# Kernel optimization log

Hardware: AMD Instinct MI355X
Metric: run time of the kernel (lower is better)

Reference implementation:

```python
import jax, jax.numpy as jnp
import numpy as np

EPS = 1e-5  # BatchNorm eps (PyTorch default)


def gcn_conv(x, edge_index, W, b):
    """PyG GCNConv with add_self_loops=True, normalize=True.
    out[j] = sum_{(i->j)} x_w[i] / sqrt(deg_i * deg_j) + x_w[j] / deg_j + b,
    deg_j = 1 + in-degree(j) (self-loop included)."""
    n = x.shape[0]
    src, dst = edge_index[0], edge_index[1]
    ones = jnp.ones(src.shape[0], x.dtype)
    deg = 1.0 + jax.ops.segment_sum(ones, dst, num_segments=n)  # [n]
    dis = jax.lax.rsqrt(deg)
    xw = x @ W  # [n, out]
    msg = xw[src] * (dis[src] * dis[dst])[:, None]  # gather + per-edge norm
    agg = jax.ops.segment_sum(msg, dst, num_segments=n)  # scatter-add
    agg = agg + xw * (1.0 / deg)[:, None]  # self-loop term
    return agg + b


def bn_relu(x, gamma, beta):
    # BatchNorm1d over the node dim (training-mode batch stats) + ReLU
    mean = x.mean(axis=0)
    var = x.var(axis=0)
    return jax.nn.relu((x - mean) * jax.lax.rsqrt(var + EPS) * gamma + beta)


def wireframe_gnn(x, edge_index, layers, fcW, fcb):
    feats = [x]
    h = x
    for (W, b, g, be) in layers:  # fixed small n_layers loop
        h = bn_relu(gcn_conv(h, edge_index, W, b), g, be)
        feats.append(h)
    cat = jnp.concatenate(feats, axis=1)
    return jax.nn.relu(cat @ fcW + fcb)


N_L, N_J = 50000, 25000
D_FC, NF = 1024, 256
E_L, E_J = 400000, 100000
L_LAB, J_LAB = 10, 3


def setup_inputs() -> dict:
    key = jax.random.key(0)
    ks = iter(jax.random.split(key, 48))
    p = lambda shape: (jax.random.normal(next(ks), shape, jnp.float32) * 0.02)
    inp = {}
    inp["line_features"] = jax.random.normal(next(ks), (N_L, D_FC), jnp.float32)
    inp["junction_features"] = jax.random.normal(next(ks), (N_J, NF), jnp.float32)
    inp["line_edge_index"] = jax.random.randint(next(ks), (2, E_L), 0, N_L, jnp.int64)
    inp["junction_edge_index"] = jax.random.randint(next(ks), (2, E_J), 0, N_J, jnp.int64)
    # line GNN: 1024 -> 512 -> 256, concat 1792 -> fc 1024
    inp["lg_W1"], inp["lg_b1"] = p((D_FC, D_FC // 2)), p((D_FC // 2,))
    inp["lg_g1"], inp["lg_be1"] = jnp.ones(D_FC // 2, jnp.float32), jnp.zeros(D_FC // 2, jnp.float32)
    inp["lg_W2"], inp["lg_b2"] = p((D_FC // 2, D_FC // 4)), p((D_FC // 4,))
    inp["lg_g2"], inp["lg_be2"] = jnp.ones(D_FC // 4, jnp.float32), jnp.zeros(D_FC // 4, jnp.float32)
    cat_l = D_FC + D_FC // 2 + D_FC // 4  # 1792
    inp["lg_fcW"], inp["lg_fcb"] = p((cat_l, D_FC)), p((D_FC,))
    # fc_lines: 1024 -> 1024 -> 1024 -> L_LAB (dim_loi*n_pts1 == dim_fc == 1024)
    inp["fl_W1"], inp["fl_b1"] = p((D_FC, D_FC)), p((D_FC,))
    inp["fl_W2"], inp["fl_b2"] = p((D_FC, D_FC)), p((D_FC,))
    inp["fl_W3"], inp["fl_b3"] = p((D_FC, L_LAB)), p((L_LAB,))
    # junction GNN: 256 -> 128 -> 64, concat 448 -> fc 256
    inp["jg_W1"], inp["jg_b1"] = p((NF, NF // 2)), p((NF // 2,))
    inp["jg_g1"], inp["jg_be1"] = jnp.ones(NF // 2, jnp.float32), jnp.zeros(NF // 2, jnp.float32)
    inp["jg_W2"], inp["jg_b2"] = p((NF // 2, NF // 4)), p((NF // 4,))
    inp["jg_g2"], inp["jg_be2"] = jnp.ones(NF // 4, jnp.float32), jnp.zeros(NF // 4, jnp.float32)
    cat_j = NF + NF // 2 + NF // 4  # 448
    inp["jg_fcW"], inp["jg_fcb"] = p((cat_j, NF)), p((NF,))
    # fc_junction: 256 -> 64 -> J_LAB
    m = NF // 4
    inp["fj_W1"], inp["fj_b1"] = p((NF, m)), p((m,))
    inp["fj_W2"], inp["fj_b2"] = p((m, J_LAB)), p((J_LAB,))
    return inp


def reference(line_features, junction_features, line_edge_index, junction_edge_index,
              lg_W1, lg_b1, lg_g1, lg_be1, lg_W2, lg_b2, lg_g2, lg_be2, lg_fcW, lg_fcb,
              fl_W1, fl_b1, fl_W2, fl_b2, fl_W3, fl_b3,
              jg_W1, jg_b1, jg_g1, jg_be1, jg_W2, jg_b2, jg_g2, jg_be2, jg_fcW, jg_fcb,
              fj_W1, fj_b1, fj_W2, fj_b2):
    # line branch
    h = wireframe_gnn(line_features, line_edge_index,
                      [(lg_W1, lg_b1, lg_g1, lg_be1), (lg_W2, lg_b2, lg_g2, lg_be2)],
                      lg_fcW, lg_fcb)
    h = jax.nn.relu(h @ fl_W1 + fl_b1)
    h = jax.nn.relu(h @ fl_W2 + fl_b2)
    line_logits = h @ fl_W3 + fl_b3
    # junction branch
    g = wireframe_gnn(junction_features, junction_edge_index,
                      [(jg_W1, jg_b1, jg_g1, jg_be1), (jg_W2, jg_b2, jg_g2, jg_be2)],
                      jg_fcW, jg_fcb)
    g = jax.nn.relu(g @ fj_W1 + fj_b1)
    junction_logits = g @ fj_W2 + fj_b2
    return (line_logits, junction_logits)
```

## Files before the change

kernel.cpp:

```cpp
#include <hip/hip_runtime.h>
#include <stdint.h>
#include <stddef.h>

typedef _Float16 f16;
typedef _Float16 f16x8 __attribute__((ext_vector_type(8)));
typedef _Float16 f16x4_t __attribute__((ext_vector_type(4)));
typedef float floatx4 __attribute__((ext_vector_type(4)));

template <int N> struct F16Vec { typedef f16 type __attribute__((ext_vector_type(N))); };

#define BN_EPS 1e-5f

struct WtJob { const float* W; f16* Wt; int K; int N; int tN; int tilebase; };
struct WtBatch { WtJob j[12]; int njobs; int ntiles; };

__global__ void k_wt_tiled(WtBatch b) {
  __shared__ float T[32][33];
  int bt = blockIdx.x;
  int i = 0;
  #pragma unroll 1
  while (i + 1 < b.njobs && bt >= b.j[i + 1].tilebase) ++i;
  WtJob J = b.j[i];
  int t = bt - J.tilebase;
  int tr = t / J.tN, tc = t - tr * J.tN;
  int ty = threadIdx.x >> 5, tx = threadIdx.x & 31;
  #pragma unroll
  for (int s = 0; s < 32; s += 8) {
    int k = tr * 32 + ty + s, n = tc * 32 + tx;
    if (k < J.K && n < J.N) T[ty + s][tx] = J.W[(size_t)k * J.N + n];
  }
  __syncthreads();
  #pragma unroll
  for (int s = 0; s < 32; s += 8) {
    int n = tc * 32 + ty + s, k = tr * 32 + tx;
    if (n < J.N && k < J.K) J.Wt[(size_t)n * J.K + k] = (f16)T[tx][ty + s];
  }
}

__global__ void k_cvt_cols(const float* __restrict__ src, f16* __restrict__ dst,
                           int n, int c, int ldd, int coff) {
  int t = blockIdx.x * blockDim.x + threadIdx.x;
  int cq = c >> 2;
  if (t >= n * cq) return;
  int r = t / cq, j = (t - r * cq) << 2;
  float4 v = *(const float4*)(src + (size_t)r * c + j);
  f16x4_t o; o[0] = (f16)v.x; o[1] = (f16)v.y; o[2] = (f16)v.z; o[3] = (f16)v.w;
  *(f16x4_t*)(dst + (size_t)r * ldd + coff + j) = o;
}

__global__ void k_count2(const int* __restrict__ dL, int EL, int* __restrict__ cntL,
                         const int* __restrict__ dJ, int EJ, int* __restrict__ cntJ) {
  int t = blockIdx.x * blockDim.x + threadIdx.x;
  if (t < EL) atomicAdd(&cntL[dL[t]], 1);
  else if (t < EL + EJ) atomicAdd(&cntJ[dJ[t - EL]], 1);
}

__global__ void k_scan4(const int* __restrict__ cnt, int n, int* __restrict__ rowstart,
                        float* __restrict__ dis) {
  __shared__ int wsum[16];
  __shared__ int carry_s;
  int tid = threadIdx.x, lane = tid & 63, wv = tid >> 6;
  if (tid == 0) { carry_s = 0; rowstart[0] = 0; }
  __syncthreads();
  for (int base = 0; base < n; base += 4096) {
    int i4 = base + tid * 4;
    int4 c = {0, 0, 0, 0};
    if (i4 < n) c = *(const int4*)(cnt + i4);
    int s0 = c.x, s1 = s0 + c.y, s2 = s1 + c.z, s3 = s2 + c.w;
    int x = s3;
    #pragma unroll
    for (int off = 1; off < 64; off <<= 1) {
      int y = __shfl_up(x, off, 64);
      if (lane >= off) x += y;
    }
    if (lane == 63) wsum[wv] = x;
    __syncthreads();
    if (wv == 0) {
      int s = (lane < 16) ? wsum[lane] : 0;
      #pragma unroll
      for (int off = 1; off < 16; off <<= 1) {
        int y = __shfl_up(s, off, 64);
        if (lane >= off) s += y;
      }
      if (lane < 16) wsum[lane] = s;
    }
    __syncthreads();
    int waveoff = (wv == 0) ? 0 : wsum[wv - 1];
    int excl = (x - s3) + waveoff + carry_s;
    if (i4 < n) {
      rowstart[i4 + 1] = excl + s0;
      rowstart[i4 + 2] = excl + s1;
      rowstart[i4 + 3] = excl + s2;
      rowstart[i4 + 4] = excl + s3;
      dis[i4 + 0] = rsqrtf(1.0f + (float)c.x);
      dis[i4 + 1] = rsqrtf(1.0f + (float)c.y);
      dis[i4 + 2] = rsqrtf(1.0f + (float)c.z);
      dis[i4 + 3] = rsqrtf(1.0f + (float)c.w);
    }
    __syncthreads();
    if (tid == 1023) carry_s = excl + s3;
    __syncthreads();
  }
}

__global__ void k_fill2(const int* __restrict__ eiL, int EL, const int* __restrict__ rsL,
                        int* __restrict__ fillL, int* __restrict__ cixL,
                        const int* __restrict__ eiJ, int EJ, const int* __restrict__ rsJ,
                        int* __restrict__ fillJ, int* __restrict__ cixJ) {
  int t = blockIdx.x * blockDim.x + threadIdx.x;
  if (t < EL) {
    int s = eiL[t], d = eiL[EL + t];
    int pos = atomicAdd(&fillL[d], 1);
    cixL[rsL[d] + pos] = s;
  } else if (t < EL + EJ) {
    int u = t - EL;
    int s = eiJ[u], d = eiJ[EJ + u];
    int pos = atomicAdd(&fillJ[d], 1);
    cixJ[rsJ[d] + pos] = s;
  }
}

template <int CPL>
__global__ void k_gather_f16(const f16* __restrict__ xw, int C,
                             const int* __restrict__ rowstart, const int* __restrict__ colidx,
                             const float* __restrict__ dis, const float* __restrict__ bias,
                             f16* __restrict__ dst, int ldd, int coff, int n) {
  typedef typename F16Vec<CPL>::type V;
  int w = threadIdx.x >> 6, l = threadIdx.x & 63;
  int j = blockIdx.x * 4 + w;
  if (j >= n) return;
  float dj = dis[j];
  int rs = rowstart[j], re = rowstart[j + 1];
  int c0 = l * CPL;
  float acc[CPL];
  {
    V p = *(const V*)(xw + (size_t)j * C + c0);
    float s = dj * dj;
    #pragma unroll
    for (int t = 0; t < CPL; ++t) acc[t] = (float)p[t] * s;
  }
  int e = rs;
  for (; e + 2 <= re; e += 2) {
    int s0 = colidx[e], s1 = colidx[e + 1];
    float f0 = dis[s0] * dj, f1 = dis[s1] * dj;
    V p0 = *(const V*)(xw + (size_t)s0 * C + c0);
    V p1 = *(const V*)(xw + (size_t)s1 * C + c0);
    #pragma unroll
    for (int t = 0; t < CPL; ++t) acc[t] += (float)p0[t] * f0 + (float)p1[t] * f1;
  }
  if (e < re) {
    int s0 = colidx[e];
    float f0 = dis[s0] * dj;
    V p0 = *(const V*)(xw + (size_t)s0 * C + c0);
    #pragma unroll
    for (int t = 0; t < CPL; ++t) acc[t] += (float)p0[t] * f0;
  }
  V o;
  #pragma unroll
  for (int t = 0; t < CPL; ++t) o[t] = (f16)(acc[t] + bias[c0 + t]);
  *(V*)(dst + (size_t)j * ldd + coff + c0) = o;
}

__global__ void k_stats(const f16* __restrict__ v, int ldd, int coff, int n, int C,
                        float* __restrict__ sum, float* __restrict__ sumsq) {
  int c = blockIdx.x * blockDim.x + threadIdx.x;
  if (c >= C) return;
  int r0 = blockIdx.y * 128, r1 = min(r0 + 128, n);
  float s = 0.f, s2 = 0.f;
  for (int r = r0; r < r1; ++r) {
    float x = (float)v[(size_t)r * ldd + coff + c];
    s += x; s2 += x * x;
  }
  atomicAdd(&sum[c], s);
  atomicAdd(&sumsq[c], s2);
}

__global__ void k_bnparam(const float* __restrict__ sum, const float* __restrict__ sumsq,
                          const float* __restrict__ gamma, const float* __restrict__ beta,
                          int n, int C, float* __restrict__ scale, float* __restrict__ shift) {
  int c = blockIdx.x * blockDim.x + threadIdx.x;
  if (c >= C) return;
  float mean = sum[c] / (float)n;
  float var = sumsq[c] / (float)n - mean * mean;
  float sc = gamma[c] * rsqrtf(var + BN_EPS);
  scale[c] = sc;
  shift[c] = beta[c] - mean * sc;
}

__global__ void k_bnapply_ip(f16* __restrict__ v, int ldd, int coff, int n, int C,
                             const float* __restrict__ scale, const float* __restrict__ shift) {
  int t = blockIdx.x * blockDim.x + threadIdx.x;
  int cq = C >> 2;
  if (t >= n * cq) return;
  int r = t / cq, c = (t - r * cq) << 2;
  f16* p = v + (size_t)r * ldd + coff + c;
  f16x4_t x = *(f16x4_t*)p;
  float4 sc = *(const float4*)(scale + c);
  float4 sh = *(const float4*)(shift + c);
  f16x4_t o;
  o[0] = (f16)fmaxf((float)x[0] * sc.x + sh.x, 0.f);
  o[1] = (f16)fmaxf((float)x[1] * sc.y + sh.y, 0.f);
  o[2] = (f16)fmaxf((float)x[2] * sc.z + sh.z, 0.f);
  o[3] = (f16)fmaxf((float)x[3] * sc.w + sh.w, 0.f);
  *(f16x4_t*)p = o;
}

__global__ __launch_bounds__(256)
void k_gemm(const f16* __restrict__ A, int lda,
            const f16* __restrict__ Bt,
            void* __restrict__ Cv, int ldc,
            const float* __restrict__ bias, int relu, int outf,
            int M, int N, int K, int mt, int nt, int per) {
  __shared__ f16 Ash[2][128 * 32];
  __shared__ f16 Bsh[2][128 * 32];
  int b = blockIdx.x;
  int g = (b & 7) * per + (b >> 3);
  if (g >= mt * nt) return;
  int tm = (g / nt) * 128, tn = (g % nt) * 128;
  int tid = threadIdx.x, l = tid & 63, w = tid >> 6;

  const f16* ag[2]; const f16* bg[2];
  uint32_t lof[2];
  #pragma unroll
  for (int j = 0; j < 2; ++j) {
    int rl = w * 32 + j * 16 + (l >> 2);
    int ck = l & 3;
    int lc = ck ^ ((rl >> 1) & 3);
    int gr = tm + rl; if (gr > M - 1) gr = M - 1;
    int gn = tn + rl; if (gn > N - 1) gn = N - 1;
    ag[j] = A + (size_t)gr * lda + lc * 8;
    bg[j] = Bt + (size_t)gn * K + lc * 8;
    lof[j] = (uint32_t)(w * 32 + j * 16) * 64;
  }

  int wm = (w >> 1) * 64, wn = (w & 1) * 64;
  int q = l >> 4, l15 = l & 15;
  uint32_t aoffb[4], boffb[4];
  #pragma unroll
  for (int i = 0; i < 4; ++i) {
    int m = wm + i * 16 + l15;
    int n2 = wn + i * 16 + l15;
    aoffb[i] = (uint32_t)(m * 32 + (q ^ ((m >> 1) & 3)) * 8) * 2;
    boffb[i] = (uint32_t)(n2 * 32 + (q ^ ((n2 >> 1) & 3)) * 8) * 2;
  }

  floatx4 acc[4][4];
  #pragma unroll
  for (int i = 0; i < 4; ++i)
    #pragma unroll
    for (int j = 0; j < 4; ++j) acc[i][j] = (floatx4){0.f, 0.f, 0.f, 0.f};

  int nk = K >> 5;
  #pragma unroll
  for (int j = 0; j < 2; ++j) {
    __builtin_amdgcn_global_load_lds(
        (const __attribute__((address_space(1))) void*)ag[j],
        (__attribute__((address_space(3))) void*)((char*)Ash + lof[j]), 16, 0, 0);
    __builtin_amdgcn_global_load_lds(
        (const __attribute__((address_space(1))) void*)bg[j],
        (__attribute__((address_space(3))) void*)((char*)Bsh + lof[j]), 16, 0, 0);
    ag[j] += 32; bg[j] += 32;
  }

  for (int i = 0; i < nk; ++i) {
    __syncthreads();
    if (i + 1 < nk) {
      uint32_t d = ((i + 1) & 1) ? 8192u : 0u;
      #pragma unroll
      for (int j = 0; j < 2; ++j) {
        __builtin_amdgcn_global_load_lds(
            (const __attribute__((address_space(1))) void*)ag[j],
            (__attribute__((address_space(3))) void*)((char*)Ash + d + lof[j]), 16, 0, 0);
        __builtin_amdgcn_global_load_lds(
            (const __attribute__((address_space(1))) void*)bg[j],
            (__attribute__((address_space(3))) void*)((char*)Bsh + d + lof[j]), 16, 0, 0);
        ag[j] += 32; bg[j] += 32;
      }
    }
    uint32_t s = (i & 1) ? 8192u : 0u;
    f16x8 af[4], bf[4];
    #pragma unroll
    for (int ii = 0; ii < 4; ++ii) {
      af[ii] = *(const f16x8*)((const char*)Ash + s + aoffb[ii]);
      bf[ii] = *(const f16x8*)((const char*)Bsh + s + boffb[ii]);
    }
    #pragma unroll
    for (int mi = 0; mi < 4; ++mi)
      #pragma unroll
      for (int ni = 0; ni < 4; ++ni)
        acc[mi][ni] = __builtin_amdgcn_mfma_f32_16x16x32_f16(af[mi], bf[ni], acc[mi][ni], 0, 0, 0);
  }

  #pragma unroll
  for (int ni = 0; ni < 4; ++ni) {
    int col = tn + wn + ni * 16 + l15;
    if (col >= N) continue;
    float bv = bias ? bias[col] : 0.f;
    #pragma unroll
    for (int mi = 0; mi < 4; ++mi) {
      int rowb = tm + wm + mi * 16 + q * 4;
      #pragma unroll
      for (int r = 0; r < 4; ++r) {
        int row = rowb + r;
        if (row < M) {
          float v = acc[mi][ni][r] + bv;
          if (relu) v = fmaxf(v, 0.f);
          if (outf) ((float*)Cv)[(size_t)row * ldc + col] = v;
          else      ((f16*)Cv)[(size_t)row * ldc + col] = (f16)v;
        }
      }
    }
  }
}

extern "C" void kernel_launch(void* const* d_in, const int* in_sizes, int n_in,
                              void* d_out, int out_size, void* d_ws, size_t ws_size,
                              hipStream_t stream) {
  (void)in_sizes; (void)n_in; (void)out_size; (void)ws_size;
  const int NL = 50000, NJ = 25000, EL = 400000, EJ = 100000;

  const float* x_l  = (const float*)d_in[0];
  const float* x_j  = (const float*)d_in[1];
  const int*   ei_l = (const int*)d_in[2];
  const int*   ei_j = (const int*)d_in[3];
  const float* lgW1 = (const float*)d_in[4];  const float* lgb1 = (const float*)d_in[5];
  const float* lgg1 = (const float*)d_in[6];  const float* lgbe1= (const float*)d_in[7];
  const float* lgW2 = (const float*)d_in[8];  const float* lgb2 = (const float*)d_in[9];
  const float* lgg2 = (const float*)d_in[10]; const float* lgbe2= (const float*)d_in[11];
  const float* lgfcW= (const float*)d_in[12]; const float* lgfcb= (const float*)d_in[13];
  const float* flW1 = (const float*)d_in[14]; const float* flb1 = (const float*)d_in[15];
  const float* flW2 = (const float*)d_in[16]; const float* flb2 = (const float*)d_in[17];
  const float* flW3 = (const float*)d_in[18]; const float* flb3 = (const float*)d_in[19];
  const float* jgW1 = (const float*)d_in[20]; const float* jgb1 = (const float*)d_in[21];
  const float* jgg1 = (const float*)d_in[22]; const float* jgbe1= (const float*)d_in[23];
  const float* jgW2 = (const float*)d_in[24]; const float* jgb2 = (const float*)d_in[25];
  const float* jgg2 = (const float*)d_in[26]; const float* jgbe2= (const float*)d_in[27];
  const float* jgfcW= (const float*)d_in[28]; const float* jgfcb= (const float*)d_in[29];
  const float* fjW1 = (const float*)d_in[30]; const float* fjb1 = (const float*)d_in[31];
  const float* fjW2 = (const float*)d_in[32]; const float* fjb2 = (const float*)d_in[33];

  char* ws = (char*)d_ws;
  size_t off = 0;
  auto alloc = [&](size_t bytes) -> char* {
    char* p = ws + off;
    off += (bytes + 255) & ~(size_t)255;
    return p;
  };

  f16* cat16 = (f16*)alloc((size_t)NL * 1792 * 2);
  f16* hA    = (f16*)alloc((size_t)NL * 1024 * 2);
  f16* hB    = (f16*)alloc((size_t)NL * 1024 * 2);
  f16*  xw16  = (f16*)hB;
  f16* catJ  = (f16*)alloc((size_t)NJ * 448 * 2);
  f16* hJA   = (f16*)alloc((size_t)NJ * 256 * 2);
  f16* hJB   = (f16*)alloc((size_t)NJ * 64 * 2);
  f16*  xwJ   = (f16*)hB;

  f16* W1t   = (f16*)alloc((size_t)1024 * 512 * 2);
  f16* W2t   = (f16*)alloc((size_t)512 * 256 * 2);
  f16* fcWt  = (f16*)alloc((size_t)1792 * 1024 * 2);
  f16* flW1t = (f16*)alloc((size_t)1024 * 1024 * 2);
  f16* flW2t = (f16*)alloc((size_t)1024 * 1024 * 2);
  f16* flW3t = (f16*)alloc((size_t)1024 * 16 * 2);
  f16* jW1t  = (f16*)alloc((size_t)256 * 128 * 2);
  f16* jW2t  = (f16*)alloc((size_t)128 * 64 * 2);
  f16* jfcWt = (f16*)alloc((size_t)448 * 256 * 2);
  f16* fjW1t = (f16*)alloc((size_t)256 * 64 * 2);
  f16* fjW2t = (f16*)alloc((size_t)64 * 4 * 2);

  int* zero0 = (int*)alloc(((size_t)2 * NL + 2 * NJ + 1920) * 4);
  int* cntL  = zero0;
  int* fillL = cntL + NL;
  int* cntJ  = fillL + NL;
  int* fillJ = cntJ + NJ;
  float* stats = (float*)(fillJ + NJ);
  float* sum1L = stats;        float* sq1L = stats + 512;
  float* sum2L = stats + 1024; float* sq2L = stats + 1280;
  float* sum1J = stats + 1536; float* sq1J = stats + 1664;
  float* sum2J = stats + 1792; float* sq2J = stats + 1856;

  int* rsL   = (int*)alloc((size_t)(NL + 4) * 4);
  int* cixL  = (int*)alloc((size_t)EL * 4);
  float* disL= (float*)alloc((size_t)NL * 4);
  int* rsJ   = (int*)alloc((size_t)(NJ + 4) * 4);
  int* cixJ  = (int*)alloc((size_t)EJ * 4);
  float* disJ= (float*)alloc((size_t)NJ * 4);
  float* scalc = (float*)alloc(512 * 4);
  float* shftc = (float*)alloc(512 * 4);

  auto cdiv = [](int a, int b) { return (a + b - 1) / b; };

  auto gemm = [&](const f16* A, int lda, const f16* Bt, void* Cc, int ldc,
                  const float* bias, int relu, int outf, int M, int N, int K) {
    int mt = cdiv(M, 128), nt = cdiv(N, 128);
    int per = cdiv(mt * nt, 8);
    k_gemm<<<8 * per, 256, 0, stream>>>(A, lda, Bt, Cc, ldc, bias, relu, outf,
                                        M, N, K, mt, nt, per);
  };
  auto bn = [&](f16* v, int ldd, int coff, int n, int C,
                float* sum, float* sumsq, const float* gamma, const float* beta) {
    dim3 gs(cdiv(C, 256), cdiv(n, 128));
    k_stats<<<gs, 256, 0, stream>>>(v, ldd, coff, n, C, sum, sumsq);
    k_bnparam<<<cdiv(C, 256), 256, 0, stream>>>(sum, sumsq, gamma, beta, n, C, scalc, shftc);
    k_bnapply_ip<<<cdiv(n * (C >> 2), 256), 256, 0, stream>>>(v, ldd, coff, n, C, scalc, shftc);
  };

  hipMemsetAsync(zero0, 0, ((size_t)2 * NL + 2 * NJ + 1920) * 4, stream);

  {
    WtBatch B2; int base = 0, nj = 0;
    auto add = [&](const float* W, f16* Wt, int K, int N) {
      int tK = cdiv(K, 32), tN = cdiv(N, 32);
      B2.j[nj++] = WtJob{W, Wt, K, N, tN, base};
      base += tK * tN;
    };
    add(lgW1, W1t, 1024, 512);
    add(lgW2, W2t, 512, 256);
    add(lgfcW, fcWt, 1792, 1024);
    add(flW1, flW1t, 1024, 1024);
    add(flW2, flW2t, 1024, 1024);
    add(flW3, flW3t, 1024, 10);
    add(jgW1, jW1t, 256, 128);
    add(jgW2, jW2t, 128, 64);
    add(jgfcW, jfcWt, 448, 256);
    add(fjW1, fjW1t, 256, 64);
    add(fjW2, fjW2t, 64, 3);
    B2.njobs = nj; B2.ntiles = base;
    k_wt_tiled<<<base, 256, 0, stream>>>(B2);
  }

  k_cvt_cols<<<cdiv(NL * 256, 256), 256, 0, stream>>>(x_l, cat16, NL, 1024, 1792, 0);
  k_cvt_cols<<<cdiv(NJ * 64, 256), 256, 0, stream>>>(x_j, catJ, NJ, 256, 448, 0);

  k_count2<<<cdiv(EL + EJ, 256), 256, 0, stream>>>(ei_l + EL, EL, cntL, ei_j + EJ, EJ, cntJ);
  k_scan4<<<1, 1024, 0, stream>>>(cntL, NL, rsL, disL);
  k_scan4<<<1, 1024, 0, stream>>>(cntJ, NJ, rsJ, disJ);
  k_fill2<<<cdiv(EL + EJ, 256), 256, 0, stream>>>(ei_l, EL, rsL, fillL, cixL,
                                                  ei_j, EJ, rsJ, fillJ, cixJ);

  gemm(cat16, 1792, W1t, xw16, 512, nullptr, 0, 0, NL, 512, 1024);
  k_gather_f16<8><<<cdiv(NL, 4), 256, 0, stream>>>(xw16, 512, rsL, cixL, disL, lgb1,
                                                   cat16, 1792, 1024, NL);
  bn(cat16, 1792, 1024, NL, 512, sum1L, sq1L, lgg1, lgbe1);

  gemm(cat16 + 1024, 1792, W2t, xw16, 256, nullptr, 0, 0, NL, 256, 512);
  k_gather_f16<4><<<cdiv(NL, 4), 256, 0, stream>>>(xw16, 256, rsL, cixL, disL, lgb2,
                                                   cat16, 1792, 1536, NL);
  bn(cat16, 1792, 1536, NL, 256, sum2L, sq2L, lgg2, lgbe2);

  gemm(cat16, 1792, fcWt, hA, 1024, lgfcb, 1, 0, NL, 1024, 1792);
  gemm(hA, 1024, flW1t, hB, 1024, flb1, 1, 0, NL, 1024, 1024);
  gemm(hB, 1024, flW2t, hA, 1024, flb2, 1, 0, NL, 1024, 1024);
  gemm(hA, 1024, flW3t, (float*)d_out, 10, flb3, 0, 1, NL, 10, 1024);

  gemm(catJ, 448, jW1t, xwJ, 128, nullptr, 0, 0, NJ, 128, 256);
  k_gather_f16<2><<<cdiv(NJ, 4), 256, 0, stream>>>(xwJ, 128, rsJ, cixJ, disJ, jgb1,
                                                   catJ, 448, 256, NJ);
  bn(catJ, 448, 256, NJ, 128, sum1J, sq1J, jgg1, jgbe1);

  gemm(catJ + 256, 448, jW2t, xwJ, 64, nullptr, 0, 0, NJ, 64, 128);
  k_gather_f16<1><<<cdiv(NJ, 4), 256, 0, stream>>>(xwJ, 64, rsJ, cixJ, disJ, jgb2,
                                                   catJ, 448, 384, NJ);
  bn(catJ, 448, 384, NJ, 64, sum2J, sq2J, jgg2, jgbe2);

  gemm(catJ, 448, jfcWt, hJA, 256, jgfcb, 1, 0, NJ, 256, 448);
  gemm(hJA, 256, fjW1t, hJB, 64, fjb1, 1, 0, NJ, 64, 256);
  gemm(hJB, 64, fjW2t, (float*)d_out + (size_t)NL * 10, 3, fjb2, 0, 1, NJ, 3, 64);
}
```

Baseline: 1.757 ms.

## Add 256x256-tile MFMA GEMM with direct global-to-LDS double-buffered pipeline

Adds a new 512-thread GEMM kernel using 256x256 output tiles, 16x16x32 f16 MFMA, XOR-swizzled LDS, and global_load_lds direct copies interleaved with MFMA phases under barrier and priority control. The dispatcher routes f16-output GEMMs with N a multiple of 256 and K a multiple of 64 to it, and keeps the old 128x128 kernel otherwise. The larger tiles raise arithmetic intensity and cut operand reloads, at the cost of 128KB of LDS per block, low occupancy, and fewer blocks for the smaller matrices. Its XCD remapping also assumes the hardware dispatches blocks round-robin across eight XCDs.

```diff
diff --git a/kernel.cpp b/kernel.cpp
--- a/kernel.cpp
+++ b/kernel.cpp
@@ -309,6 +309,151 @@
           else      ((f16*)Cv)[(size_t)row * ldc + col] = (f16)v;
         }
       }
+    }
+  }
+}
+
+#define G_BAR()   __builtin_amdgcn_s_barrier()
+#define G_LGKM0() asm volatile("s_waitcnt lgkmcnt(0)" ::: "memory")
+
+#define MFMA_PHASE(NI, B0v, B1v)                                              \
+  __builtin_amdgcn_s_setprio(1);                                              \
+  _Pragma("unroll")                                                           \
+  for (int mi = 0; mi < 8; ++mi) {                                            \
+    acc[mi][NI] = __builtin_amdgcn_mfma_f32_16x16x32_f16(B0v, af[mi][0], acc[mi][NI], 0, 0, 0); \
+    acc[mi][NI] = __builtin_amdgcn_mfma_f32_16x16x32_f16(B1v, af[mi][1], acc[mi][NI], 0, 0, 0); \
+  }                                                                           \
+  __builtin_amdgcn_s_setprio(0);
+
+__global__ __launch_bounds__(512, 2)
+void k_gemm256(const f16* __restrict__ A, int lda,
+               const f16* __restrict__ Bt,
+               f16* __restrict__ C, int ldc,
+               const float* __restrict__ bias, int relu,
+               int M, int N, int K, int mt, int nt) {
+  __shared__ char lds[131072];
+  char* ldsc = (char*)lds;
+  int nwg = mt * nt;
+  int b = blockIdx.x;
+  int xcd = b & 7, lid = b >> 3;
+  int q8 = nwg >> 3, r8 = nwg & 7;
+  int wg = (xcd < r8 ? xcd * (q8 + 1) : r8 * (q8 + 1) + (xcd - r8) * q8) + lid;
+  int tm = (wg / nt) * 256, tn = (wg % nt) * 256;
+  int tid = threadIdx.x, l = tid & 63, w = tid >> 6;
+  int wm = w >> 2, wn = w & 3;
+  int q = l >> 4, l15 = l & 15;
+  int nk = K >> 6;
+
+  int r0 = tid >> 3, r1 = r0 + 64;
+  int ck = (tid & 7) ^ (r0 & 7);
+  int gmA0a = tm + r0;        if (gmA0a > M - 1) gmA0a = M - 1;
+  int gmA0b = tm + r1;        if (gmA0b > M - 1) gmA0b = M - 1;
+  int gmA1a = tm + 128 + r0;  if (gmA1a > M - 1) gmA1a = M - 1;
+  int gmA1b = tm + 128 + r1;  if (gmA1b > M - 1) gmA1b = M - 1;
+  int gnB0a = tn + r0;        if (gnB0a > N - 1) gnB0a = N - 1;
+  int gnB0b = tn + r1;        if (gnB0b > N - 1) gnB0b = N - 1;
+  int gnB1a = tn + 128 + r0;  if (gnB1a > N - 1) gnB1a = N - 1;
+  int gnB1b = tn + 128 + r1;  if (gnB1b > N - 1) gnB1b = N - 1;
+  const f16* pA0a = A + (size_t)gmA0a * lda + ck * 8;
+  const f16* pA0b = A + (size_t)gmA0b * lda + ck * 8;
+  const f16* pA1a = A + (size_t)gmA1a * lda + ck * 8;
+  const f16* pA1b = A + (size_t)gmA1b * lda + ck * 8;
+  const f16* pB0a = Bt + (size_t)gnB0a * K + ck * 8;
+  const f16* pB0b = Bt + (size_t)gnB0b * K + ck * 8;
+  const f16* pB1a = Bt + (size_t)gnB1a * K + ck * 8;
+  const f16* pB1b = Bt + (size_t)gnB1b * K + ck * 8;
+  uint32_t dst0 = (uint32_t)tid * 16;
+
+  auto ST2 = [&](const f16*& pa, const f16*& pb, uint32_t dst) {
+    __builtin_amdgcn_global_load_lds(
+        (const __attribute__((address_space(1))) void*)pa,
+        (__attribute__((address_space(3))) void*)(ldsc + dst), 16, 0, 0);
+    __builtin_amdgcn_global_load_lds(
+        (const __attribute__((address_space(1))) void*)pb,
+        (__attribute__((address_space(3))) void*)(ldsc + dst + 8192), 16, 0, 0);
+    pa += 64; pb += 64;
+  };
+  auto SA0 = [&](uint32_t bb) { ST2(pA0a, pA0b, bb + dst0); };
+  auto SA1 = [&](uint32_t bb) { ST2(pA1a, pA1b, bb + 16384u + dst0); };
+  auto SB0 = [&](uint32_t bb) { ST2(pB0a, pB0b, bb + 32768u + dst0); };
+  auto SB1 = [&](uint32_t bb) { ST2(pB1a, pB1b, bb + 49152u + dst0); };
+
+  uint32_t abase = (uint32_t)((wm * 128 + l15) * 128);
+  uint32_t bbase = (uint32_t)(32768 + (wn * 64 + l15) * 128);
+  uint32_t cof0 = (uint32_t)(((0 + q) ^ (l15 & 7)) * 16);
+  uint32_t cof1 = (uint32_t)(((4 + q) ^ (l15 & 7)) * 16);
+
+  floatx4 acc[8][4];
+  #pragma unroll
+  for (int i = 0; i < 8; ++i)
+    #pragma unroll
+    for (int j = 0; j < 4; ++j) acc[i][j] = (floatx4){0.f, 0.f, 0.f, 0.f};
+
+  SA0(0u); SA1(0u); SB0(0u); SB1(0u);
+  if (nk > 1) { SA0(65536u); SA1(65536u); SB0(65536u); }
+  asm volatile("s_waitcnt vmcnt(6)" ::: "memory");
+  G_BAR();
+
+  f16x8 af[8][2];
+  for (int t = 0; t < nk; ++t) {
+    uint32_t cb = (t & 1) ? 65536u : 0u;
+    uint32_t ob = 65536u - cb;
+    const char* cbp = ldsc + cb;
+    if (t + 1 < nk) SB1(ob);
+    #pragma unroll
+    for (int mi = 0; mi < 8; ++mi) {
+      af[mi][0] = *(const f16x8*)(cbp + abase + mi * 2048 + cof0);
+      af[mi][1] = *(const f16x8*)(cbp + abase + mi * 2048 + cof1);
+    }
+    f16x8 b00 = *(const f16x8*)(cbp + bbase + cof0);
+    f16x8 b01 = *(const f16x8*)(cbp + bbase + cof1);
+    G_BAR(); G_LGKM0();
+    MFMA_PHASE(0, b00, b01);
+    G_BAR();
+    if (t + 2 < nk) SA0(cb);
+    f16x8 b10 = *(const f16x8*)(cbp + bbase + 2048 + cof0);
+    f16x8 b11 = *(const f16x8*)(cbp + bbase + 2048 + cof1);
+    G_BAR(); G_LGKM0();
+    MFMA_PHASE(1, b10, b11);
+    G_BAR();
+    if (t + 2 < nk) SA1(cb);
+    f16x8 b20 = *(const f16x8*)(cbp + bbase + 4096 + cof0);
+    f16x8 b21 = *(const f16x8*)(cbp + bbase + 4096 + cof1);
+    f16x8 b30 = *(const f16x8*)(cbp + bbase + 6144 + cof0);
+    f16x8 b31 = *(const f16x8*)(cbp + bbase + 6144 + cof1);
+    G_BAR(); G_LGKM0();
+    MFMA_PHASE(2, b20, b21);
+    G_BAR();
+    if (t + 2 < nk) {
+      SB0(cb);
+      asm volatile("s_waitcnt vmcnt(6)" ::: "memory");
+    } else {
+      asm volatile("s_waitcnt vmcnt(0)" ::: "memory");
+    }
+    G_BAR();
+    MFMA_PHASE(3, b30, b31);
+  }
+
+  #pragma unroll
+  for (int mi = 0; mi < 8; ++mi) {
+    int m = tm + wm * 128 + mi * 16 + l15;
+    if (m >= M) continue;
+    f16* crow = C + (size_t)m * ldc;
+    #pragma unroll
+    for (int ni = 0; ni < 4; ++ni) {
+      int n0 = tn + wn * 64 + ni * 16 + q * 4;
+      floatx4 v = acc[mi][ni];
+      if (bias) {
+        float4 bv = *(const float4*)(bias + n0);
+        v[0] += bv.x; v[1] += bv.y; v[2] += bv.z; v[3] += bv.w;
+      }
+      if (relu) {
+        v[0] = fmaxf(v[0], 0.f); v[1] = fmaxf(v[1], 0.f);
+        v[2] = fmaxf(v[2], 0.f); v[3] = fmaxf(v[3], 0.f);
+      }
+      f16x4_t o;
+      o[0] = (f16)v[0]; o[1] = (f16)v[1]; o[2] = (f16)v[2]; o[3] = (f16)v[3];
+      *(f16x4_t*)(crow + n0) = o;
     }
   }
 }
@@ -392,10 +537,16 @@
 
   auto gemm = [&](const f16* A, int lda, const f16* Bt, void* Cc, int ldc,
                   const float* bias, int relu, int outf, int M, int N, int K) {
-    int mt = cdiv(M, 128), nt = cdiv(N, 128);
-    int per = cdiv(mt * nt, 8);
-    k_gemm<<<8 * per, 256, 0, stream>>>(A, lda, Bt, Cc, ldc, bias, relu, outf,
-                                        M, N, K, mt, nt, per);
+    if (!outf && (N & 255) == 0 && N >= 256 && (K & 63) == 0 && K >= 128) {
+      int mt = cdiv(M, 256), nt = N >> 8;
+      k_gemm256<<<mt * nt, 512, 0, stream>>>(A, lda, Bt, (f16*)Cc, ldc, bias, relu,
+                                             M, N, K, mt, nt);
+    } else {
+      int mt = cdiv(M, 128), nt = cdiv(N, 128);
+      int per = cdiv(mt * nt, 8);
+      k_gemm<<<8 * per, 256, 0, stream>>>(A, lda, Bt, Cc, ldc, bias, relu, outf,
+                                          M, N, K, mt, nt, per);
+    }
   };
   auto bn = [&](f16* v, int ldd, int coff, int n, int C,
                 float* sum, float* sumsq, const float* gamma, const float* beta) {
```

Result: faster. 1.507 ms (-14.2%).
